# Kernel optimization log

Measured on AMD Instinct MI355X. Metric: run time of the kernel, lower is better.

## Reference

```python
import jax, jax.numpy as jnp
import numpy as np

W_SIZE = 5      # temporal_window_size
N_SUBSETS = 3   # graph adjacency subsets
PAD = (W_SIZE - 1) // 2
BN_EPS = 1e-5


def setup_inputs() -> dict:
    key = jax.random.key(0)
    k1, k2, k3, k4 = jax.random.split(key, 4)
    B, Cin, T, V = 32, 96, 288, 25
    Cout = 96
    x = jax.random.normal(k1, (B, Cin, T, V), dtype=jnp.float32)
    A = jax.random.uniform(k2, (N_SUBSETS, V, V), dtype=jnp.float32)
    conv_w = jax.random.normal(k3, (N_SUBSETS * Cout, Cin), dtype=jnp.float32) * 0.05
    conv_b = jax.random.normal(k4, (N_SUBSETS * Cout,), dtype=jnp.float32) * 0.05
    gamma = jnp.ones((Cout,), dtype=jnp.float32)
    beta = jnp.zeros((Cout,), dtype=jnp.float32)
    return {"x": x, "A": A, "conv_w": conv_w, "conv_b": conv_b,
            "gamma": gamma, "beta": beta}


def reference(x, A, conv_w, conv_b, gamma, beta):
    # x: (B, Cin, T, V); A: (S, V, V); conv_w: (S*Cout, Cin)
    B, Cin, T, V = x.shape
    S = N_SUBSETS
    Cout = conv_w.shape[0] // S

    # 1x1 conv: (B, S*Cout, T, V)
    y = jnp.einsum('bitv,oi->botv', x, conv_w) + conv_b[None, :, None, None]
    y = y.reshape(B, S, Cout, T, V)

    # Graph aggregation fused over subsets. The torch code tiles A along the
    # window axis and einsums 'bscfn,snm->bcfm' over the unfolded tensor; that
    # is mathematically (1/W) * sum_k sum_s sum_n y[b,s,c,f+k-pad,n] A[s,n,m].
    # Aggregate spatially first (sum over s and n), then window-sum in time.
    z = jnp.einsum('bsctn,snm->bctm', y, A)  # (B, Cout, T, V)

    # Temporal window sum with zero padding (stride=1, dilation=1).
    zp = jnp.pad(z, ((0, 0), (0, 0), (PAD, PAD), (0, 0)))
    out = zp[:, :, 0:T, :]
    for k in range(1, W_SIZE):
        out = out + zp[:, :, k:k + T, :]
    out = out * (1.0 / W_SIZE)

    # BatchNorm2d (training-mode batch statistics over B, T, V per channel)
    mean = jnp.mean(out, axis=(0, 2, 3), keepdims=True)
    var = jnp.var(out, axis=(0, 2, 3), keepdims=True)
    out = (out - mean) * jax.lax.rsqrt(var + BN_EPS)
    out = out * gamma[None, :, None, None] + beta[None, :, None, None]

    return jax.nn.relu(out)
```

## Files before the change

kernel.cpp:

```cpp
#include <hip/hip_runtime.h>
#include <hip/hip_bf16.h>

#define BB 32
#define CIN 96
#define TT 288
#define VV 25
#define SS 3
#define COUT 96
#define WSZ 5
#define BN_EPS 1e-5f
#define TV (TT*VV)
#define KK 288
#define XCOLS 64

typedef __attribute__((ext_vector_type(8))) short bf16x8;
typedef __attribute__((ext_vector_type(4))) float f32x4;

__device__ __forceinline__ unsigned short f2bf(float f) {
    unsigned u = __float_as_uint(f);
    return (unsigned short)((u + 0x7fffu + ((u >> 16) & 1u)) >> 16);
}

__global__ __launch_bounds__(256) void prep(
    const float* __restrict__ conv_w, const float* __restrict__ A,
    const float* __restrict__ cb,
    __hip_bfloat16* __restrict__ Wflat,
    __hip_bfloat16* __restrict__ Bfr,
    float* __restrict__ zbias,
    float* __restrict__ stats)
{
    int id = blockIdx.x*256 + threadIdx.x;
    if (id < 27648) {
        int c = id / KK, k = id - c*KK;
        int s = k / CIN, i = k - s*CIN;
        Wflat[id] = __float2bfloat16(0.2f * conv_w[(s*COUT + c)*CIN + i]);
    } else if (id < 27648 + 3072) {
        int e = id - 27648;
        int f = e >> 9, rem = e & 511;
        int l = rem >> 3, j = rem & 7;
        int s = f >> 1, nt = f & 1;
        int n = (l >> 4)*8 + j;
        int m = nt*16 + (l & 15);
        float v = (n < VV && m < VV) ? A[(s*VV + n)*VV + m] : 0.0f;
        Bfr[e] = __float2bfloat16(v);
    } else if (id < 27648 + 3072 + 2400) {
        int e = id - 27648 - 3072;
        int c = e / VV, m = e - c*VV;
        float v = 0.f;
        #pragma unroll
        for (int s = 0; s < SS; ++s) {
            float sa = 0.f;
            #pragma unroll
            for (int n = 0; n < VV; ++n) sa += A[(s*VV + n)*VV + m];
            v = fmaf(cb[s*COUT + c], sa, v);
        }
        zbias[e] = v;
    } else if (id < 27648 + 3072 + 2400 + 192) {
        stats[id - 27648 - 3072 - 2400] = 0.0f;
    }
}

__global__ __launch_bounds__(256) void fused(
    const float* __restrict__ x,
    const __hip_bfloat16* __restrict__ Wflat,
    const __hip_bfloat16* __restrict__ Bfr,
    const float* __restrict__ zbias,
    float* __restrict__ out)
{
    __shared__ __hip_bfloat16 XAt[XCOLS*KK];
    const int tid  = threadIdx.x;
    const int lane = tid & 63;
    const int wave = tid >> 6;
    const int quad = lane >> 4;
    const int lrow = lane & 15;
    const int tile = blockIdx.x;
    const int b    = blockIdx.y;
    const int t0   = tile*2;

    bf16x8 bf1[6];
    #pragma unroll
    for (int f = 0; f < 6; ++f)
        bf1[f] = *(const bf16x8*)(Bfr + (f*64 + lane)*8);

    #pragma unroll
    for (int mt3 = 0; mt3 < 3; ++mt3) {
        const int Mtile = wave*3 + mt3;
        const int arow = Mtile*16 + lrow;
        const int ai = arow >> 1, atl = arow & 1;
        const int t  = t0 + atl;
        const float* xr = x + ((size_t)(b*CIN + ai)*TT + t)*VV;
        float xv[8];
        #pragma unroll
        for (int j = 0; j < 8; ++j) xv[j] = 0.f;
        if (quad < 3) {
            #pragma unroll
            for (int dt = -2; dt <= 2; ++dt) {
                if ((unsigned)(t + dt) < TT) {
                    #pragma unroll
                    for (int j = 0; j < 8; ++j) xv[j] += xr[dt*VV + quad*8 + j];
                }
            }
        } else {
            #pragma unroll
            for (int dt = -2; dt <= 2; ++dt)
                if ((unsigned)(t + dt) < TT) xv[0] += xr[dt*VV + 24];
        }
        bf16x8 af;
        #pragma unroll
        for (int j = 0; j < 8; ++j) ((short*)&af)[j] = (short)f2bf(xv[j]);

        const int i0 = Mtile*8 + quad*2;
        #pragma unroll
        for (int s = 0; s < SS; ++s) {
            #pragma unroll
            for (int nt = 0; nt < 2; ++nt) {
                f32x4 d = {0.f, 0.f, 0.f, 0.f};
                d = __builtin_amdgcn_mfma_f32_16x16x32_bf16(af, bf1[s*2+nt], d, 0, 0, 0);
                const int m = nt*16 + lrow;
                if (m < VV) {
                    const int k0 = s*CIN + i0;
                    const int g  = k0 >> 3, o = k0 & 7;
                    #pragma unroll
                    for (int tl = 0; tl < 2; ++tl) {
                        const int col = tl*VV + m;
                        const int gs  = (g & ~3) | ((g & 3) ^ ((col >> 1) & 3));
                        unsigned int pv = (unsigned int)f2bf(d[tl])
                                        | ((unsigned int)f2bf(d[tl+2]) << 16);
                        ((unsigned int*)XAt)[(col*KK + gs*8 + o) >> 1] = pv;
                    }
                }
            }
        }
    }
    __syncthreads();

    const int mh = wave & 1, nh = wave >> 1;
    f32x4 acc[3][2] = {};
    for (int it = 0; it < 9; ++it) {
        const int k0 = it*32;
        bf16x8 bfrag[2];
        #pragma unroll
        for (int ct = 0; ct < 2; ++ct) {
            const int cl = (nh*2 + ct)*16 + lrow;
            const int g0 = it*4 + (quad ^ ((cl >> 1) & 3));
            bfrag[ct] = *(const bf16x8*)&XAt[cl*KK + g0*8];
        }
        #pragma unroll
        for (int mt = 0; mt < 3; ++mt) {
            const int c = (mh*3 + mt)*16 + lrow;
            bf16x8 afrag = *(const bf16x8*)(Wflat + c*KK + k0 + quad*8);
            #pragma unroll
            for (int ct = 0; ct < 2; ++ct)
                acc[mt][ct] = __builtin_amdgcn_mfma_f32_16x16x32_bf16(
                    afrag, bfrag[ct], acc[mt][ct], 0, 0, 0);
        }
    }

    #pragma unroll
    for (int ct = 0; ct < 2; ++ct) {
        const int cl = (nh*2 + ct)*16 + lrow;
        if (cl < 2*VV) {
            const int tl = (cl >= VV) ? 1 : 0;
            const int m  = cl - tl*VV;
            const int t  = t0 + tl;
            const int lo = (t-2 < 0) ? 0 : t-2;
            const int hi = (t+2 > TT-1) ? TT-1 : t+2;
            const float zs = (float)(hi - lo + 1) * 0.2f;
            float* obase = out + ((size_t)b*COUT*TT + t)*VV + m;
            #pragma unroll
            for (int mt = 0; mt < 3; ++mt) {
                const int cbase = (mh*3 + mt)*16 + quad*4;
                #pragma unroll
                for (int r = 0; r < 4; ++r) {
                    const int c = cbase + r;
                    obase[(size_t)c*TV] = acc[mt][ct][r] + zbias[c*VV + m] * zs;
                }
            }
        }
    }
}

__global__ __launch_bounds__(256) void k2_stats(
    const float* __restrict__ zbuf, float* __restrict__ ssum, float* __restrict__ ssq)
{
    __shared__ float red[8];
    const int tid  = threadIdx.x;
    const int slab = blockIdx.x;
    const int c    = slab % COUT;
    const float4* s4 = (const float4*)(zbuf + (size_t)slab * TV);
    float ls = 0.f, ls2 = 0.f;
    for (int e = tid; e < TV/4; e += 256) {
        float4 v = s4[e];
        ls  += (v.x + v.y) + (v.z + v.w);
        ls2 = fmaf(v.x, v.x, ls2);
        ls2 = fmaf(v.y, v.y, ls2);
        ls2 = fmaf(v.z, v.z, ls2);
        ls2 = fmaf(v.w, v.w, ls2);
    }
    #pragma unroll
    for (int off = 32; off > 0; off >>= 1) {
        ls  += __shfl_down(ls,  off, 64);
        ls2 += __shfl_down(ls2, off, 64);
    }
    const int lane = tid & 63, wid = tid >> 6;
    if (lane == 0) { red[wid*2] = ls; red[wid*2+1] = ls2; }
    __syncthreads();
    if (tid == 0) {
        atomicAdd(&ssum[c], red[0] + red[2] + red[4] + red[6]);
        atomicAdd(&ssq[c],  red[1] + red[3] + red[5] + red[7]);
    }
}

__global__ __launch_bounds__(256) void k4_norm(
    float* __restrict__ buf, const float* __restrict__ ssum, const float* __restrict__ ssq,
    const float* __restrict__ gamma, const float* __restrict__ beta)
{
    const int tid  = threadIdx.x;
    const int slab = blockIdx.x;
    const int c    = slab % COUT;
    const float invN = 1.0f / (float)(BB * TV);
    const float mean = ssum[c] * invN;
    const float var  = ssq[c] * invN - mean * mean;
    const float inv  = rsqrtf(var + BN_EPS);
    const float sc   = gamma[c] * inv;
    const float bi   = beta[c] - mean * sc;
    float4* p = (float4*)(buf + (size_t)slab * TV);
    for (int u = tid; u < TV/4; u += 256) {
        float4 v = p[u];
        v.x = fmaxf(fmaf(v.x, sc, bi), 0.0f);
        v.y = fmaxf(fmaf(v.y, sc, bi), 0.0f);
        v.z = fmaxf(fmaf(v.z, sc, bi), 0.0f);
        v.w = fmaxf(fmaf(v.w, sc, bi), 0.0f);
        p[u] = v;
    }
}

extern "C" void kernel_launch(void* const* d_in, const int* in_sizes, int n_in,
                              void* d_out, int out_size, void* d_ws, size_t ws_size,
                              hipStream_t stream) {
    const float* x      = (const float*)d_in[0];
    const float* A      = (const float*)d_in[1];
    const float* conv_w = (const float*)d_in[2];
    const float* conv_b = (const float*)d_in[3];
    const float* gamma  = (const float*)d_in[4];
    const float* beta   = (const float*)d_in[5];
    float* out = (float*)d_out;

    float* zbias = (float*)d_ws;
    float* ssum  = zbias + 2400;
    float* ssq   = ssum + COUT;
    __hip_bfloat16* Wflat = (__hip_bfloat16*)(ssq + COUT);
    __hip_bfloat16* Bfr   = Wflat + (size_t)COUT * KK;

    prep    <<<dim3(131),        dim3(256), 0, stream>>>(conv_w, A, conv_b, Wflat, Bfr, zbias, ssum);
    fused   <<<dim3(TT/2, BB),   dim3(256), 0, stream>>>(x, Wflat, Bfr, zbias, out);
    k2_stats<<<dim3(BB*COUT),    dim3(256), 0, stream>>>(out, ssum, ssq);
    k4_norm <<<dim3(BB*COUT),    dim3(256), 0, stream>>>(out, ssum, ssq, gamma, beta);
}
```

Before: 312.0 us.

## Fuse BatchNorm statistics into GEMM epilogue and drop separate stats pass

Computes per-channel sum and sum-of-squares in the fused kernel's epilogue, reducing across lanes with shuffles, then through shared-memory atomics, then one global atomic per channel per block. The standalone stats kernel, which re-read the whole output buffer, is removed. It also remaps blockIdx.x to interleave time tiles, probably to spread L2/channel access. The cost is extra register pressure in the epilogue and many global atomics on 192 addresses.

```diff
diff --git a/kernel.cpp b/kernel.cpp
--- a/kernel.cpp
+++ b/kernel.cpp
@@ -65,17 +65,22 @@
     const __hip_bfloat16* __restrict__ Wflat,
     const __hip_bfloat16* __restrict__ Bfr,
     const float* __restrict__ zbias,
-    float* __restrict__ out)
+    float* __restrict__ out,
+    float* __restrict__ stats)
 {
     __shared__ __hip_bfloat16 XAt[XCOLS*KK];
+    __shared__ float sh_stats[192];
     const int tid  = threadIdx.x;
     const int lane = tid & 63;
     const int wave = tid >> 6;
     const int quad = lane >> 4;
     const int lrow = lane & 15;
-    const int tile = blockIdx.x;
+    const int px   = blockIdx.x;
+    const int tile = ((px & 7) * 18) + (px >> 3);
     const int b    = blockIdx.y;
     const int t0   = tile*2;
+
+    if (tid < 192) sh_stats[tid] = 0.0f;
 
     bf16x8 bf1[6];
     #pragma unroll
@@ -156,6 +161,10 @@
         }
     }
 
+    float ps[12], pq[12];
+    #pragma unroll
+    for (int i = 0; i < 12; ++i) { ps[i] = 0.f; pq[i] = 0.f; }
+
     #pragma unroll
     for (int ct = 0; ct < 2; ++ct) {
         const int cl = (nh*2 + ct)*16 + lrow;
@@ -173,54 +182,45 @@
                 #pragma unroll
                 for (int r = 0; r < 4; ++r) {
                     const int c = cbase + r;
-                    obase[(size_t)c*TV] = acc[mt][ct][r] + zbias[c*VV + m] * zs;
+                    const float v = acc[mt][ct][r] + zbias[c*VV + m] * zs;
+                    obase[(size_t)c*TV] = v;
+                    ps[mt*4 + r] += v;
+                    pq[mt*4 + r] = fmaf(v, v, pq[mt*4 + r]);
                 }
             }
         }
     }
-}
-
-__global__ __launch_bounds__(256) void k2_stats(
-    const float* __restrict__ zbuf, float* __restrict__ ssum, float* __restrict__ ssq)
-{
-    __shared__ float red[8];
-    const int tid  = threadIdx.x;
-    const int slab = blockIdx.x;
-    const int c    = slab % COUT;
-    const float4* s4 = (const float4*)(zbuf + (size_t)slab * TV);
-    float ls = 0.f, ls2 = 0.f;
-    for (int e = tid; e < TV/4; e += 256) {
-        float4 v = s4[e];
-        ls  += (v.x + v.y) + (v.z + v.w);
-        ls2 = fmaf(v.x, v.x, ls2);
-        ls2 = fmaf(v.y, v.y, ls2);
-        ls2 = fmaf(v.z, v.z, ls2);
-        ls2 = fmaf(v.w, v.w, ls2);
-    }
-    #pragma unroll
-    for (int off = 32; off > 0; off >>= 1) {
-        ls  += __shfl_down(ls,  off, 64);
-        ls2 += __shfl_down(ls2, off, 64);
-    }
-    const int lane = tid & 63, wid = tid >> 6;
-    if (lane == 0) { red[wid*2] = ls; red[wid*2+1] = ls2; }
+
+    #pragma unroll
+    for (int off = 1; off < 16; off <<= 1) {
+        #pragma unroll
+        for (int i = 0; i < 12; ++i) {
+            ps[i] += __shfl_xor(ps[i], off, 64);
+            pq[i] += __shfl_xor(pq[i], off, 64);
+        }
+    }
+    if (lrow == 0) {
+        #pragma unroll
+        for (int i = 0; i < 12; ++i) {
+            const int c = (mh*3 + (i >> 2))*16 + quad*4 + (i & 3);
+            atomicAdd(&sh_stats[c],      ps[i]);
+            atomicAdd(&sh_stats[96 + c], pq[i]);
+        }
+    }
     __syncthreads();
-    if (tid == 0) {
-        atomicAdd(&ssum[c], red[0] + red[2] + red[4] + red[6]);
-        atomicAdd(&ssq[c],  red[1] + red[3] + red[5] + red[7]);
-    }
+    if (tid < 192) atomicAdd(&stats[tid], sh_stats[tid]);
 }
 
 __global__ __launch_bounds__(256) void k4_norm(
-    float* __restrict__ buf, const float* __restrict__ ssum, const float* __restrict__ ssq,
+    float* __restrict__ buf, const float* __restrict__ stats,
     const float* __restrict__ gamma, const float* __restrict__ beta)
 {
     const int tid  = threadIdx.x;
     const int slab = blockIdx.x;
     const int c    = slab % COUT;
     const float invN = 1.0f / (float)(BB * TV);
-    const float mean = ssum[c] * invN;
-    const float var  = ssq[c] * invN - mean * mean;
+    const float mean = stats[c] * invN;
+    const float var  = stats[96 + c] * invN - mean * mean;
     const float inv  = rsqrtf(var + BN_EPS);
     const float sc   = gamma[c] * inv;
     const float bi   = beta[c] - mean * sc;
@@ -247,13 +247,11 @@
     float* out = (float*)d_out;
 
     float* zbias = (float*)d_ws;
-    float* ssum  = zbias + 2400;
-    float* ssq   = ssum + COUT;
-    __hip_bfloat16* Wflat = (__hip_bfloat16*)(ssq + COUT);
+    float* stats = zbias + 2400;
+    __hip_bfloat16* Wflat = (__hip_bfloat16*)(stats + 192);
     __hip_bfloat16* Bfr   = Wflat + (size_t)COUT * KK;
 
-    prep    <<<dim3(131),        dim3(256), 0, stream>>>(conv_w, A, conv_b, Wflat, Bfr, zbias, ssum);
-    fused   <<<dim3(TT/2, BB),   dim3(256), 0, stream>>>(x, Wflat, Bfr, zbias, out);
-    k2_stats<<<dim3(BB*COUT),    dim3(256), 0, stream>>>(out, ssum, ssq);
-    k4_norm <<<dim3(BB*COUT),    dim3(256), 0, stream>>>(out, ssum, ssq, gamma, beta);
-}
+    prep   <<<dim3(131),      dim3(256), 0, stream>>>(conv_w, A, conv_b, Wflat, Bfr, zbias, stats);
+    fused  <<<dim3(TT/2, BB), dim3(256), 0, stream>>>(x, Wflat, Bfr, zbias, out, stats);
+    k4_norm<<<dim3(BB*COUT),  dim3(256), 0, stream>>>(out, stats, gamma, beta);
+}
```

Result: no change. 310.7 us (-0.4%).
